# Kernel tuning notes

Measured on AMD Instinct MI355X. Metric: run time of the kernel, lower is better.

Reference implementation:

```python
import jax, jax.numpy as jnp
import numpy as np

N_HEAD = 16
LN_EPS = 1e-5


def _layernorm(x, g, b):
    mu = jnp.mean(x, axis=-1, keepdims=True)
    var = jnp.mean(jnp.square(x - mu), axis=-1, keepdims=True)
    return (x - mu) * jax.lax.rsqrt(var + LN_EPS) * g + b


def setup_inputs() -> dict:
    key = jax.random.key(0)
    ks = jax.random.split(key, 8)
    B, T, C = 2, 2048, 1024
    Dff = 4 * C
    s = 0.02
    return {
        "x": jax.random.normal(ks[0], (B, T, C), jnp.float32),
        "wq": jax.random.normal(ks[1], (C, C), jnp.float32) * s,
        "wk": jax.random.normal(ks[2], (C, C), jnp.float32) * s,
        "wv": jax.random.normal(ks[3], (C, C), jnp.float32) * s,
        "w_proj": jax.random.normal(ks[4], (C, C), jnp.float32) * s,
        "b_proj": jnp.zeros((C,), jnp.float32),
        "w1": jax.random.normal(ks[5], (C, Dff), jnp.float32) * s,
        "b1": jnp.zeros((Dff,), jnp.float32),
        "w2": jax.random.normal(ks[6], (Dff, C), jnp.float32) * s,
        "b2": jnp.zeros((C,), jnp.float32),
        "g1": jnp.ones((C,), jnp.float32),
        "be1": jnp.zeros((C,), jnp.float32),
        "g2": jnp.ones((C,), jnp.float32),
        "be2": jnp.zeros((C,), jnp.float32),
    }


def reference(x, wq, wk, wv, w_proj, b_proj, w1, b1, w2, b2, g1, be1, g2, be2):
    B, T, C = x.shape
    H = N_HEAD
    hd = C // H
    # QKV projections (all heads folded into one matmul each), -> [B,H,T,hd]
    q = (x @ wq).reshape(B, T, H, hd).transpose(0, 2, 1, 3)
    k = (x @ wk).reshape(B, T, H, hd).transpose(0, 2, 1, 3)
    v = (x @ wv).reshape(B, T, H, hd).transpose(0, 2, 1, 3)
    # scaled causal attention; scale = head_size ** -0.5 as in torch source
    scores = jnp.einsum("bhqd,bhkd->bhqk", q, k) * (hd ** -0.5)
    causal = jnp.tril(jnp.ones((T, T), bool))
    scores = jnp.where(causal, scores, jnp.finfo(scores.dtype).min)
    wei = jax.nn.softmax(scores, axis=-1)
    attn = jnp.einsum("bhqk,bhkd->bhqd", wei, v)  # [B,H,T,hd]
    attn = attn.transpose(0, 2, 1, 3).reshape(B, T, C)
    y = attn @ w_proj + b_proj
    # post-LN residuals as in Block.forward
    x = _layernorm(x + y, g1, be1)
    y = jnp.maximum(x @ w1 + b1, 0.0) @ w2 + b2
    x = _layernorm(x + y, g2, be2)
    return x
```

## Files before the change

### kernel.cpp

```cpp
#include <hip/hip_runtime.h>
#include <hip/hip_bf16.h>


typedef __attribute__((ext_vector_type(8))) short bf16x8;
typedef __attribute__((ext_vector_type(4))) float f32x4;
typedef __attribute__((ext_vector_type(4))) short short4v;

__device__ inline short f2bf(float f) {
    __hip_bfloat16 h = __float2bfloat16(f);
    return *reinterpret_cast<short*>(&h);
}
__device__ inline float bf2f(short s) {
    union { unsigned u; float f; } c;
    c.u = ((unsigned)(unsigned short)s) << 16;
    return c.f;
}

__global__ __launch_bounds__(256) void mega_prep(const float* __restrict__ x,
                                                 short* __restrict__ x_bf,
                                                 const float* __restrict__ wq,
                                                 const float* __restrict__ wk,
                                                 const float* __restrict__ wv,
                                                 const float* __restrict__ wp,
                                                 short* __restrict__ wqT,
                                                 short* __restrict__ wkT,
                                                 short* __restrict__ wvT,
                                                 short* __restrict__ wpT,
                                                 const float* __restrict__ w1,
                                                 short* __restrict__ w1T,
                                                 const float* __restrict__ w2,
                                                 short* __restrict__ w2T,
                                                 float scaleq) {
    const int blk = blockIdx.x;
    const int tid = threadIdx.x;
    if (blk < 4096) {
        const int i = blk * 256 + tid;
        float4 v = *(const float4*)(x + (size_t)i * 4);
        short4v o = { f2bf(v.x), f2bf(v.y), f2bf(v.z), f2bf(v.w) };
        *(short4v*)(x_bf + (size_t)i * 4) = o;
        return;
    }
    __shared__ short tile[32][33];
    const int tx = tid & 31, ty = tid >> 5;
    const float* in;
    short* out;
    int R, C, bx, by;
    float scale = 1.0f;
    if (blk < 8192) {
        const int b2 = blk - 4096;
        const int z = b2 >> 10;
        const int rem = b2 & 1023;
        bx = rem & 31; by = rem >> 5;
        R = 1024; C = 1024;
        in = z == 0 ? wq : z == 1 ? wk : z == 2 ? wv : wp;
        out = z == 0 ? wqT : z == 1 ? wkT : z == 2 ? wvT : wpT;
        if (z == 0) scale = scaleq;
    } else if (blk < 12288) {
        const int rem = blk - 8192;
        bx = rem & 127; by = rem >> 7;
        R = 1024; C = 4096;
        in = w1; out = w1T;
    } else {
        const int rem = blk - 12288;
        bx = rem & 31; by = rem >> 5;
        R = 4096; C = 1024;
        in = w2; out = w2T;
    }
    const int c0 = bx * 32, r0 = by * 32;
    for (int i = ty; i < 32; i += 8)
        tile[i][tx] = f2bf(in[(size_t)(r0 + i) * C + c0 + tx] * scale);
    __syncthreads();
    for (int i = ty; i < 32; i += 8)
        out[(size_t)(c0 + i) * R + r0 + tx] = tile[tx][i];
}

#define STAGE256(KT, ASB, BSB)                                                              \
    do {                                                                                    \
        const int kof_ = (KT) * 64;                                                         \
        _Pragma("unroll") for (int l = 0; l < 4; ++l) {                                     \
            const int ch = wid * 4 + l;                                                     \
            const short* ga = A + (size_t)(row0 + ch * 8 + sr) * lda + kof_ + scs;          \
            __builtin_amdgcn_global_load_lds(                                               \
                (const __attribute__((address_space(1))) unsigned int*)ga,                  \
                (__attribute__((address_space(3))) unsigned int*)((ASB) + ch * 512), 16, 0, 0); \
            const short* gb = BT + (size_t)(col0 + ch * 8 + sr) * ldb + kof_ + scs;         \
            __builtin_amdgcn_global_load_lds(                                               \
                (const __attribute__((address_space(1))) unsigned int*)gb,                  \
                (__attribute__((address_space(3))) unsigned int*)((BSB) + ch * 512), 16, 0, 0); \
        }                                                                                   \
    } while (0)

template <int BIAS, int RELU>
__device__ __forceinline__ void gemm256_core(const short* __restrict__ A,
                                             const short* __restrict__ BT,
                                             const float* __restrict__ bias,
                                             short* __restrict__ C,
                                             int N, int K, int lda, int ldb,
                                             int row0, int col0, bool addbias,
                                             short* As0, short* As1,
                                             short* Bs0, short* Bs1) {
    const int tid = threadIdx.x;
    const int wid = tid >> 6;
    const int lane = tid & 63;
    const int wm = wid >> 2;
    const int wn = wid & 3;
    const int lr = lane & 15;
    const int lk = (lane >> 4) * 8;
    const int sr = lane >> 3;
    const int scs = ((lane & 7) * 8) ^ (sr * 8);
    const int rsw = (lr & 7) * 8;

    f32x4 acc[8][4] = {};
    STAGE256(0, As0, Bs0);
    STAGE256(1, As1, Bs1);

    const int NK = K >> 6;
#pragma unroll 1
    for (int t = 0; t < NK; ++t) {
        short* Asc = (t & 1) ? As1 : As0;
        short* Bsc = (t & 1) ? Bs1 : Bs0;
        if (t == NK - 1)
            asm volatile("s_waitcnt vmcnt(0)" ::: "memory");
        else
            asm volatile("s_waitcnt vmcnt(8)" ::: "memory");
        __builtin_amdgcn_s_barrier();
        bf16x8 bfr[4][2];
#pragma unroll
        for (int fj = 0; fj < 4; ++fj)
#pragma unroll
            for (int ks = 0; ks < 2; ++ks)
                bfr[fj][ks] = *(const bf16x8*)(&Bsc[(wn * 64 + fj * 16 + lr) * 64 +
                                                    ((ks * 32 + lk) ^ rsw)]);
#pragma unroll
        for (int p = 0; p < 4; ++p) {
            bf16x8 afr[2][2];
#pragma unroll
            for (int f = 0; f < 2; ++f)
#pragma unroll
                for (int ks = 0; ks < 2; ++ks)
                    afr[f][ks] = *(const bf16x8*)(&Asc[(wm * 128 + (p * 2 + f) * 16 + lr) * 64 +
                                                       ((ks * 32 + lk) ^ rsw)]);
            asm volatile("s_waitcnt lgkmcnt(0)" ::: "memory");
            __builtin_amdgcn_sched_barrier(0);
            if (p == 3) {
                __builtin_amdgcn_s_barrier();
                if (t + 2 < NK) STAGE256(t + 2, Asc, Bsc);
            }
            __builtin_amdgcn_s_setprio(1);
#pragma unroll
            for (int f = 0; f < 2; ++f)
#pragma unroll
                for (int fj = 0; fj < 4; ++fj)
#pragma unroll
                    for (int ks = 0; ks < 2; ++ks)
                        acc[p * 2 + f][fj] = __builtin_amdgcn_mfma_f32_16x16x32_bf16(
                            afr[f][ks], bfr[fj][ks], acc[p * 2 + f][fj], 0, 0, 0);
            __builtin_amdgcn_s_setprio(0);
            __builtin_amdgcn_s_barrier();
        }
    }
#pragma unroll
    for (int fi = 0; fi < 8; ++fi) {
        const int row = row0 + wm * 128 + fi * 16 + (lane >> 4) * 4;
#pragma unroll
        for (int fj = 0; fj < 4; ++fj) {
            const int col = col0 + wn * 64 + fj * 16 + lr;
            const float bv = (BIAS && addbias) ? bias[col] : 0.0f;
#pragma unroll
            for (int r = 0; r < 4; ++r) {
                float v = acc[fi][fj][r] + bv;
                if (RELU) v = fmaxf(v, 0.0f);
                C[(size_t)(row + r) * N + col] = f2bf(v);
            }
        }
    }
}

__global__ __launch_bounds__(512, 2) void gemm_mlp1(const short* __restrict__ A,
                                                    const short* __restrict__ BT,
                                                    const float* __restrict__ bias,
                                                    short* __restrict__ C) {
    __shared__ short As[2][256 * 64];
    __shared__ short Bs[2][256 * 64];
    const int flat = blockIdx.x;
    const int w = (flat & 7) * 32 + (flat >> 3);
    const int row0 = (w & 15) * 256;
    const int col0 = (w >> 4) * 256;
    gemm256_core<1, 1>(A, BT, bias, C, 4096, 1024, 1024, 1024, row0, col0, true,
                       As[0], As[1], Bs[0], Bs[1]);
}

__global__ __launch_bounds__(512, 2) void gemm_qkvvt(const short* __restrict__ x_bf,
                                                     const short* __restrict__ wqkT,
                                                     const short* __restrict__ wvT,
                                                     short* __restrict__ qk,
                                                     short* __restrict__ Vt) {
    __shared__ short As[2][256 * 64];
    __shared__ short Bs[2][256 * 64];
    int flat = blockIdx.x;
    if (flat < 128) {
        const int w = (flat & 7) * 16 + (flat >> 3);
        const int row0 = (w & 15) * 256;
        const int col0 = (w >> 4) * 256;
        gemm256_core<0, 0>(x_bf, wqkT, nullptr, qk, 2048, 1024, 1024, 1024,
                           row0, col0, false, As[0], As[1], Bs[0], Bs[1]);
    } else {
        flat -= 128;
        const int w = (flat & 7) * 8 + (flat >> 3);
        const int row0 = (w & 3) * 256;
        const int col0 = (w >> 2) * 256;
        gemm256_core<0, 0>(wvT, x_bf, nullptr, Vt, 4096, 1024, 1024, 1024,
                           row0, col0, false, As[0], As[1], Bs[0], Bs[1]);
    }
}

__global__ __launch_bounds__(512, 2) void gemm_z4(const short* __restrict__ A,
                                                  const short* __restrict__ BT,
                                                  const float* __restrict__ bias,
                                                  short* __restrict__ C0,
                                                  short* __restrict__ C1,
                                                  short* __restrict__ C2,
                                                  short* __restrict__ C3,
                                                  int Kz, int lda, int ldb) {
    __shared__ short As[2][256 * 64];
    __shared__ short Bs[2][256 * 64];
    const int kz = blockIdx.z;
    short* C = kz == 0 ? C0 : kz == 1 ? C1 : kz == 2 ? C2 : C3;
    const int flat = blockIdx.x;
    const int w = (flat & 7) * 8 + (flat >> 3);
    const int row0 = (w & 15) * 256;
    const int col0 = (w >> 4) * 256;
    gemm256_core<1, 0>(A + kz * Kz, BT + kz * Kz, bias, C, 1024, Kz,
                       lda, ldb, row0, col0, kz == 0, As[0], As[1], Bs[0], Bs[1]);
}

#define ATT_T 2048
#define ATT_QKS 2048
#define ATT_BT 4096

#define LOADK(KF, KB)                                                                     \
    do {                                                                                  \
        const int k0_ = (KB) * 64;                                                        \
        _Pragma("unroll") for (int t = 0; t < 4; ++t) {                                   \
            const size_t krow_ = (size_t)(b * ATT_T + k0_ + 16 * t + lr) * ATT_QKS + h * 64; \
            KF[t][0] = *(const bf16x8*)(Km + krow_ + g * 8);                              \
            KF[t][1] = *(const bf16x8*)(Km + krow_ + 32 + g * 8);                         \
        }                                                                                 \
    } while (0)

#define LOADV(VF, KB)                                                                     \
    do {                                                                                  \
        const int k0_ = (KB) * 64;                                                        \
        _Pragma("unroll") for (int n = 0; n < 4; ++n)                                     \
            _Pragma("unroll") for (int ks = 0; ks < 2; ++ks)                              \
                VF[n][ks] = *(const bf16x8*)(Vt + (size_t)(h * 64 + n * 16 + lr) * ATT_BT + \
                                             b * ATT_T + k0_ + ks * 32 + g * 8);          \
    } while (0)

#define COMPUTE(KF, VF, KB)                                                               \
    do {                                                                                  \
        const int k0_ = (KB) * 64;                                                        \
        const bool edge_ = (KB) == nfull;                                                 \
        _Pragma("unroll") for (int qs = 0; qs < 2; ++qs) {                                \
            f32x4 st[4];                                                                  \
            __builtin_amdgcn_s_setprio(1);                                                \
            _Pragma("unroll") for (int t = 0; t < 4; ++t) {                               \
                f32x4 s = {};                                                             \
                s = __builtin_amdgcn_mfma_f32_16x16x32_bf16(KF[t][0], aq[qs][0], s, 0, 0, 0); \
                s = __builtin_amdgcn_mfma_f32_16x16x32_bf16(KF[t][1], aq[qs][1], s, 0, 0, 0); \
                st[t] = s;                                                                \
            }                                                                             \
            __builtin_amdgcn_s_setprio(0);                                                \
            float rst[4];                                                                 \
            _Pragma("unroll") for (int t = 0; t < 4; ++t) {                               \
                short4v pw;                                                               \
                float pr[4];                                                              \
                _Pragma("unroll") for (int r = 0; r < 4; ++r) {                           \
                    float val = st[t][r];                                                 \
                    if (edge_ && (k0_ + 16 * t + g * 4 + r > qrow[qs])) val = -3e38f;     \
                    float p = exp2f(val);                                                 \
                    pr[r] = p;                                                            \
                    pw[r] = f2bf(p);                                                      \
                }                                                                         \
                rst[t] = (pr[0] + pr[1]) + (pr[2] + pr[3]);                               \
                *(short4v*)(&Plds[wid][qs][lr][16 * t + g * 4]) = pw;                     \
            }                                                                             \
            float rs = (rst[0] + rst[1]) + (rst[2] + rst[3]);                             \
            rs += __shfl_xor(rs, 16);                                                     \
            rs += __shfl_xor(rs, 32);                                                     \
            lrun[qs] += rs;                                                               \
        }                                                                                 \
        asm volatile("s_waitcnt lgkmcnt(0)" ::: "memory");                                \
        __builtin_amdgcn_sched_barrier(0);                                                \
        __builtin_amdgcn_s_setprio(1);                                                    \
        _Pragma("unroll") for (int qs = 0; qs < 2; ++qs)                                  \
            _Pragma("unroll") for (int ks = 0; ks < 2; ++ks) {                            \
                bf16x8 pf = *(const bf16x8*)(&Plds[wid][qs][lr][ks * 32 + g * 8]);        \
                _Pragma("unroll") for (int n = 0; n < 4; ++n)                             \
                    O[qs][n] = __builtin_amdgcn_mfma_f32_16x16x32_bf16(VF[n][ks], pf, O[qs][n], 0, 0, 0); \
            }                                                                             \
        __builtin_amdgcn_s_setprio(0);                                                    \
    } while (0)

__global__ __launch_bounds__(128) void flash_attn(const short* __restrict__ Q,
                                                  const short* __restrict__ Km,
                                                  const short* __restrict__ Vt,
                                                  short* __restrict__ Oout) {
    const int f = blockIdx.x;
    const int wid = threadIdx.x >> 6;
    const int lane = threadIdx.x & 63;
    const int lr = lane & 15;
    const int g = lane >> 4;
    const int xcd = f & 7;
    const int k = f >> 3;
    const int bh = xcd * 4 + (k & 3);
    const int b = bh >> 4;
    const int h = bh & 15;
    const int pair = (k >> 2) * 2 + wid;

    __shared__ __align__(16) short Plds[2][2][16][72];

#pragma unroll 1
    for (int job = 0; job < 2; ++job) {
        const int s = job ? (63 - pair) : pair;
        const int q0 = s << 5;
        const int qrow[2] = { q0 + lr, q0 + 16 + lr };
        const int nfull = s >> 1;

        bf16x8 aq[2][2];
#pragma unroll
        for (int qs = 0; qs < 2; ++qs)
#pragma unroll
            for (int ds = 0; ds < 2; ++ds)
                aq[qs][ds] = *(const bf16x8*)(Q + (size_t)(b * ATT_T + q0 + qs * 16 + lr) * ATT_QKS +
                                              h * 64 + ds * 32 + g * 8);

        f32x4 O[2][4] = {};
        float lrun[2] = { 0.0f, 0.0f };

        bf16x8 kfA[4][2], kfB[4][2], vf[4][2];
        LOADK(kfA, 0);
        int kb = 0;
        while (true) {
            LOADV(vf, kb);
            if (kb < nfull) LOADK(kfB, kb + 1);
            COMPUTE(kfA, vf, kb);
            ++kb;
            if (kb > nfull) break;
            LOADV(vf, kb);
            if (kb < nfull) LOADK(kfA, kb + 1);
            COMPUTE(kfB, vf, kb);
            ++kb;
            if (kb > nfull) break;
        }

#pragma unroll
        for (int qs = 0; qs < 2; ++qs) {
            const float inv = 1.0f / lrun[qs];
#pragma unroll
            for (int n = 0; n < 4; ++n) {
                short4v ov;
#pragma unroll
                for (int r = 0; r < 4; ++r) ov[r] = f2bf(O[qs][n][r] * inv);
                *(short4v*)(Oout + (size_t)(b * ATT_T + q0 + qs * 16 + lr) * 1024 +
                            h * 64 + n * 16 + g * 4) = ov;
            }
        }
    }
}

template <int XB>
__global__ __launch_bounds__(256) void resid_ln(const float* __restrict__ xf,
                                                const short* __restrict__ xb,
                                                const short* __restrict__ y,
                                                const short* __restrict__ yb,
                                                const short* __restrict__ yc,
                                                const short* __restrict__ yd,
                                                const float* __restrict__ g,
                                                const float* __restrict__ be,
                                                float* __restrict__ of,
                                                short* __restrict__ ob) {
    const int row = blockIdx.x;
    const int tid = threadIdx.x;
    const size_t base = (size_t)row * 1024 + tid * 4;
    float x0, x1, x2, x3;
    if (XB) {
        short4v xv = *(const short4v*)(xb + base);
        x0 = bf2f(xv[0]); x1 = bf2f(xv[1]); x2 = bf2f(xv[2]); x3 = bf2f(xv[3]);
    } else {
        float4 xv = *(const float4*)(xf + base);
        x0 = xv.x; x1 = xv.y; x2 = xv.z; x3 = xv.w;
    }
    short4v yv = *(const short4v*)(y + base);
    float h0 = x0 + bf2f(yv[0]), h1 = x1 + bf2f(yv[1]);
    float h2 = x2 + bf2f(yv[2]), h3 = x3 + bf2f(yv[3]);
    if (yb) {
        short4v v2 = *(const short4v*)(yb + base);
        h0 += bf2f(v2[0]); h1 += bf2f(v2[1]); h2 += bf2f(v2[2]); h3 += bf2f(v2[3]);
    }
    if (yc) {
        short4v v3 = *(const short4v*)(yc + base);
        h0 += bf2f(v3[0]); h1 += bf2f(v3[1]); h2 += bf2f(v3[2]); h3 += bf2f(v3[3]);
    }
    if (yd) {
        short4v v4 = *(const short4v*)(yd + base);
        h0 += bf2f(v4[0]); h1 += bf2f(v4[1]); h2 += bf2f(v4[2]); h3 += bf2f(v4[3]);
    }
    float s = h0 + h1 + h2 + h3;
    float ss = h0 * h0 + h1 * h1 + h2 * h2 + h3 * h3;
#pragma unroll
    for (int d = 1; d < 64; d <<= 1) {
        s += __shfl_xor(s, d);
        ss += __shfl_xor(ss, d);
    }
    __shared__ float as_[4], ass_[4];
    if ((tid & 63) == 0) { as_[tid >> 6] = s; ass_[tid >> 6] = ss; }
    __syncthreads();
    s = as_[0] + as_[1] + as_[2] + as_[3];
    ss = ass_[0] + ass_[1] + ass_[2] + ass_[3];
    const float mu = s * (1.0f / 1024.0f);
    const float var = ss * (1.0f / 1024.0f) - mu * mu;
    const float rstd = rsqrtf(var + 1e-5f);
    float4 gv = *(const float4*)(g + tid * 4);
    float4 bv = *(const float4*)(be + tid * 4);
    float o0 = (h0 - mu) * rstd * gv.x + bv.x;
    float o1 = (h1 - mu) * rstd * gv.y + bv.y;
    float o2 = (h2 - mu) * rstd * gv.z + bv.z;
    float o3 = (h3 - mu) * rstd * gv.w + bv.w;
    if (of) {
        float4 ov = { o0, o1, o2, o3 };
        *(float4*)(of + base) = ov;
    }
    if (ob) {
        short4v obv = { f2bf(o0), f2bf(o1), f2bf(o2), f2bf(o3) };
        *(short4v*)(ob + base) = obv;
    }
}


extern "C" void kernel_launch(void* const* d_in, const int* in_sizes, int n_in,
                              void* d_out, int out_size, void* d_ws, size_t ws_size,
                              hipStream_t stream) {
    const float* x = (const float*)d_in[0];
    const float* wq = (const float*)d_in[1];
    const float* wk = (const float*)d_in[2];
    const float* wv = (const float*)d_in[3];
    const float* wp = (const float*)d_in[4];
    const float* bproj = (const float*)d_in[5];
    const float* w1 = (const float*)d_in[6];
    const float* b1 = (const float*)d_in[7];
    const float* w2 = (const float*)d_in[8];
    const float* b2 = (const float*)d_in[9];
    const float* g1 = (const float*)d_in[10];
    const float* be1 = (const float*)d_in[11];
    const float* g2 = (const float*)d_in[12];
    const float* be2 = (const float*)d_in[13];

    char* ws = (char*)d_ws;
    const size_t MB = 1024 * 1024;
    short* x_bf = (short*)(ws + 0);
    short* wqkT = (short*)(ws + 8 * MB);
    short* wqT = wqkT;
    short* wkT = (short*)(ws + 10 * MB);
    short* wvT = (short*)(ws + 12 * MB);
    short* w1T = (short*)(ws + 16 * MB);
    short* w2T = (short*)(ws + 24 * MB);
    short* qk  = (short*)(ws + 32 * MB);
    short* wpT = (short*)(ws + 48 * MB);
    short* Vt  = (short*)(ws + 56 * MB);
    short* hbf = (short*)(ws + 32 * MB);
    short* attn = (short*)(ws + 64 * MB);
    short* x1bf = (short*)(ws + 64 * MB);
    short* y1a = (short*)(ws + 72 * MB);
    short* y1b = (short*)(ws + 0);
    short* y1c = (short*)(ws + 8 * MB);
    short* y1d = (short*)(ws + 88 * MB);
    short* y2a = (short*)(ws + 72 * MB);
    short* y2b = (short*)(ws + 0);
    short* y2c = (short*)(ws + 8 * MB);
    short* y2d = (short*)(ws + 16 * MB);

    dim3 blk(256);
    const float SC = 0.125f * 1.44269504089f;

    mega_prep<<<dim3(16384), blk, 0, stream>>>(x, x_bf, wq, wk, wv, wp,
                                               wqT, wkT, wvT, wpT,
                                               w1, w1T, w2, w2T, SC);
    gemm_qkvvt<<<dim3(192), dim3(512), 0, stream>>>(x_bf, wqkT, wvT, qk, Vt);
    flash_attn<<<dim3(512), dim3(128), 0, stream>>>(qk, qk + 1024, Vt, attn);
    gemm_z4<<<dim3(64, 1, 4), dim3(512), 0, stream>>>(attn, wpT, bproj,
                                                      y1a, y1b, y1c, y1d, 256, 1024, 1024);
    resid_ln<0><<<dim3(4096), blk, 0, stream>>>(x, nullptr, y1a, y1b, y1c, y1d,
                                                g1, be1, nullptr, x1bf);
    gemm_mlp1<<<dim3(256), dim3(512), 0, stream>>>(x1bf, w1T, b1, hbf);
    gemm_z4<<<dim3(64, 1, 4), dim3(512), 0, stream>>>(hbf, w2T, b2,
                                                      y2a, y2b, y2c, y2d, 1024, 4096, 4096);
    resid_ln<1><<<dim3(4096), blk, 0, stream>>>(nullptr, x1bf, y2a, y2b, y2c, y2d,
                                                g2, be2, (float*)d_out, nullptr);
}
```

Before: 251.9 us.

## Overlap weight transposes with attention and feed bf16 input to first residual

The up-front prep kernel now only converts x and transposes the Q/K/V weights. The w_proj, w1 and w2 bf16 transposes are appended as 9216 extra blocks of the flash-attention launch, so they can run on CUs left idle by the 512 attention blocks instead of delaying the QKV GEMM. The first residual+LayerNorm now reads the bf16 copy of x rather than the fp32 original, cutting its read traffic at some cost in residual precision. Workspace buffers are relocated so x_bf stays live until that LayerNorm runs.

```diff
diff --git a/kernel.cpp b/kernel.cpp
--- a/kernel.cpp
+++ b/kernel.cpp
@@ -16,21 +16,15 @@
     return c.f;
 }
 
-__global__ __launch_bounds__(256) void mega_prep(const float* __restrict__ x,
-                                                 short* __restrict__ x_bf,
-                                                 const float* __restrict__ wq,
-                                                 const float* __restrict__ wk,
-                                                 const float* __restrict__ wv,
-                                                 const float* __restrict__ wp,
-                                                 short* __restrict__ wqT,
-                                                 short* __restrict__ wkT,
-                                                 short* __restrict__ wvT,
-                                                 short* __restrict__ wpT,
-                                                 const float* __restrict__ w1,
-                                                 short* __restrict__ w1T,
-                                                 const float* __restrict__ w2,
-                                                 short* __restrict__ w2T,
-                                                 float scaleq) {
+__global__ __launch_bounds__(256) void prep_a(const float* __restrict__ x,
+                                              short* __restrict__ x_bf,
+                                              const float* __restrict__ wq,
+                                              const float* __restrict__ wk,
+                                              const float* __restrict__ wv,
+                                              short* __restrict__ wqT,
+                                              short* __restrict__ wkT,
+                                              short* __restrict__ wvT,
+                                              float scaleq) {
     const int blk = blockIdx.x;
     const int tid = threadIdx.x;
     if (blk < 4096) {
@@ -42,36 +36,19 @@
     }
     __shared__ short tile[32][33];
     const int tx = tid & 31, ty = tid >> 5;
-    const float* in;
-    short* out;
-    int R, C, bx, by;
-    float scale = 1.0f;
-    if (blk < 8192) {
-        const int b2 = blk - 4096;
-        const int z = b2 >> 10;
-        const int rem = b2 & 1023;
-        bx = rem & 31; by = rem >> 5;
-        R = 1024; C = 1024;
-        in = z == 0 ? wq : z == 1 ? wk : z == 2 ? wv : wp;
-        out = z == 0 ? wqT : z == 1 ? wkT : z == 2 ? wvT : wpT;
-        if (z == 0) scale = scaleq;
-    } else if (blk < 12288) {
-        const int rem = blk - 8192;
-        bx = rem & 127; by = rem >> 7;
-        R = 1024; C = 4096;
-        in = w1; out = w1T;
-    } else {
-        const int rem = blk - 12288;
-        bx = rem & 31; by = rem >> 5;
-        R = 4096; C = 1024;
-        in = w2; out = w2T;
-    }
+    const int b2 = blk - 4096;
+    const int z = b2 >> 10;
+    const int rem = b2 & 1023;
+    const int bx = rem & 31, by = rem >> 5;
+    const float* in = z == 0 ? wq : z == 1 ? wk : wv;
+    short* out = z == 0 ? wqT : z == 1 ? wkT : wvT;
+    const float scale = z == 0 ? scaleq : 1.0f;
     const int c0 = bx * 32, r0 = by * 32;
     for (int i = ty; i < 32; i += 8)
-        tile[i][tx] = f2bf(in[(size_t)(r0 + i) * C + c0 + tx] * scale);
+        tile[i][tx] = f2bf(in[(size_t)(r0 + i) * 1024 + c0 + tx] * scale);
     __syncthreads();
     for (int i = ty; i < 32; i += 8)
-        out[(size_t)(c0 + i) * R + r0 + tx] = tile[tx][i];
+        out[(size_t)(c0 + i) * 1024 + r0 + tx] = tile[tx][i];
 }
 
 #define STAGE256(KT, ASB, BSB)                                                              \
@@ -305,10 +282,41 @@
 __global__ __launch_bounds__(128) void flash_attn(const short* __restrict__ Q,
                                                   const short* __restrict__ Km,
                                                   const short* __restrict__ Vt,
-                                                  short* __restrict__ Oout) {
+                                                  short* __restrict__ Oout,
+                                                  const float* __restrict__ wp,
+                                                  const float* __restrict__ w1,
+                                                  const float* __restrict__ w2,
+                                                  short* __restrict__ wpT,
+                                                  short* __restrict__ w1T,
+                                                  short* __restrict__ w2T) {
     const int f = blockIdx.x;
-    const int wid = threadIdx.x >> 6;
-    const int lane = threadIdx.x & 63;
+    const int tid = threadIdx.x;
+    if (f >= 512) {
+        __shared__ short tile[32][33];
+        int t = f - 512;
+        const float* in;
+        short* out;
+        int Rr, Cc, bx, by;
+        if (t < 1024) {
+            in = wp; out = wpT; Rr = 1024; Cc = 1024; bx = t & 31; by = t >> 5;
+        } else if (t < 5120) {
+            const int r = t - 1024;
+            in = w1; out = w1T; Rr = 1024; Cc = 4096; bx = r & 127; by = r >> 7;
+        } else {
+            const int r = t - 5120;
+            in = w2; out = w2T; Rr = 4096; Cc = 1024; bx = r & 31; by = r >> 5;
+        }
+        const int tx = tid & 31, ty = tid >> 5;
+        const int c0 = bx * 32, r0 = by * 32;
+        for (int i = ty; i < 32; i += 4)
+            tile[i][tx] = f2bf(in[(size_t)(r0 + i) * Cc + c0 + tx]);
+        __syncthreads();
+        for (int i = ty; i < 32; i += 4)
+            out[(size_t)(c0 + i) * Rr + r0 + tx] = tile[tx][i];
+        return;
+    }
+    const int wid = tid >> 6;
+    const int lane = tid & 63;
     const int lr = lane & 15;
     const int g = lane >> 4;
     const int xcd = f & 7;
@@ -472,8 +480,8 @@
     short* attn = (short*)(ws + 64 * MB);
     short* x1bf = (short*)(ws + 64 * MB);
     short* y1a = (short*)(ws + 72 * MB);
-    short* y1b = (short*)(ws + 0);
-    short* y1c = (short*)(ws + 8 * MB);
+    short* y1b = (short*)(ws + 32 * MB);
+    short* y1c = (short*)(ws + 40 * MB);
     short* y1d = (short*)(ws + 88 * MB);
     short* y2a = (short*)(ws + 72 * MB);
     short* y2b = (short*)(ws + 0);
@@ -483,14 +491,13 @@
     dim3 blk(256);
     const float SC = 0.125f * 1.44269504089f;
 
-    mega_prep<<<dim3(16384), blk, 0, stream>>>(x, x_bf, wq, wk, wv, wp,
-                                               wqT, wkT, wvT, wpT,
-                                               w1, w1T, w2, w2T, SC);
+    prep_a<<<dim3(7168), blk, 0, stream>>>(x, x_bf, wq, wk, wv, wqT, wkT, wvT, SC);
     gemm_qkvvt<<<dim3(192), dim3(512), 0, stream>>>(x_bf, wqkT, wvT, qk, Vt);
-    flash_attn<<<dim3(512), dim3(128), 0, stream>>>(qk, qk + 1024, Vt, attn);
+    flash_attn<<<dim3(9728), dim3(128), 0, stream>>>(qk, qk + 1024, Vt, attn,
+                                                     wp, w1, w2, wpT, w1T, w2T);
     gemm_z4<<<dim3(64, 1, 4), dim3(512), 0, stream>>>(attn, wpT, bproj,
                                                       y1a, y1b, y1c, y1d, 256, 1024, 1024);
-    resid_ln<0><<<dim3(4096), blk, 0, stream>>>(x, nullptr, y1a, y1b, y1c, y1d,
+    resid_ln<1><<<dim3(4096), blk, 0, stream>>>(nullptr, x_bf, y1a, y1b, y1c, y1d,
                                                 g1, be1, nullptr, x1bf);
     gemm_mlp1<<<dim3(256), dim3(512), 0, stream>>>(x1bf, w1T, b1, hbf);
     gemm_z4<<<dim3(64, 1, 4), dim3(512), 0, stream>>>(hbf, w2T, b2,
```

Result: slower. 295.8 us (+17.4%).
